# Performance work log

Measured on AMD Instinct MI355X. Metric: run time of the kernel, lower is better.

The kernel has to match this reference:

```python
import jax, jax.numpy as jnp
import numpy as np

N_NODES = 50000
N_EDGES = 800000
D_IN = 128
D_OUT = 128


def setup_inputs() -> dict:
    key = jax.random.key(0)
    k1, k2, k3, k4, k5 = jax.random.split(key, 5)
    x = jax.random.normal(k1, (N_NODES, D_IN), dtype=jnp.float32)
    w = jax.random.normal(k2, (D_IN, D_OUT), dtype=jnp.float32) * (1.0 / np.sqrt(D_IN))
    adj_rows = jnp.sort(jax.random.randint(k3, (N_EDGES,), 0, N_NODES, dtype=jnp.int32))
    adj_cols = jax.random.randint(k4, (N_EDGES,), 0, N_NODES, dtype=jnp.int32)
    adj_vals = jax.random.uniform(k5, (N_EDGES,), dtype=jnp.float32)
    return {"x": x, "w": w, "adj_rows": adj_rows, "adj_cols": adj_cols, "adj_vals": adj_vals}


def reference(x, w, adj_rows, adj_cols, adj_vals):
    # dense feature transform: [N, D_in] @ [D_in, D_out] -> [N, D_out]
    h = jnp.matmul(x, w)
    # sparse adjacency propagation (SpMM in COO form):
    # out[r] = sum over edges (r, c, v) of v * h[c]
    msg = adj_vals[:, None] * h[adj_cols]          # [E, D_out] gather
    out = jax.ops.segment_sum(msg, adj_rows, num_segments=x.shape[0])
    # activation (relu), fused into output pass
    return jax.nn.relu(out)
```

## Files before the change

### kernel.cpp

```cpp
#include <hip/hip_runtime.h>
#include <hip/hip_bf16.h>

#define D 128
#define GEMM_ROWS 32

typedef __bf16 bf16x8 __attribute__((ext_vector_type(8)));
typedef float  f32x4  __attribute__((ext_vector_type(4)));
typedef unsigned int u32x4 __attribute__((ext_vector_type(4)));

__global__ void transpose_w(const float* __restrict__ w, unsigned short* __restrict__ wT) {
    int idx = blockIdx.x * 256 + threadIdx.x;
    float v = w[idx];
    int k = idx >> 7, c = idx & 127;
    wT[c * D + k] = __builtin_bit_cast(unsigned short, (__bf16)v);
}

__global__ void build_row_ptr(const int* __restrict__ rows, int* __restrict__ row_ptr,
                              int n_edges, int n_nodes) {
    int e = blockIdx.x * 256 + threadIdx.x;
    if (e >= n_edges) return;
    int r    = rows[e];
    int prev = (e == 0) ? -1 : rows[e - 1];
    for (int rr = prev + 1; rr <= r; ++rr) row_ptr[rr] = e;
    if (e == n_edges - 1)
        for (int rr = r + 1; rr <= n_nodes; ++rr) row_ptr[rr] = n_edges;
}

__device__ inline bf16x8 load_a_frag(const float* __restrict__ x, int r, int koff, int n) {
    float4 v0 = make_float4(0.f, 0.f, 0.f, 0.f), v1 = v0;
    if (r < n) {
        const float4* p = (const float4*)(x + (size_t)r * D + koff);
        v0 = p[0]; v1 = p[1];
    }
    bf16x8 a;
    a[0] = (__bf16)v0.x; a[1] = (__bf16)v0.y; a[2] = (__bf16)v0.z; a[3] = (__bf16)v0.w;
    a[4] = (__bf16)v1.x; a[5] = (__bf16)v1.y; a[6] = (__bf16)v1.z; a[7] = (__bf16)v1.w;
    return a;
}

__global__ __launch_bounds__(256) void gemm_mfma2(const float* __restrict__ x,
                                                  const unsigned short* __restrict__ wT,
                                                  unsigned short* __restrict__ h, int n) {
    const int wave = threadIdx.x >> 6;
    const int lane = threadIdx.x & 63;
    const int m16  = lane & 15;
    const int q    = lane >> 4;

    const int row0 = blockIdx.x * 64;
    const int col0 = wave * 32;

    const u32x4* wTv = (const u32x4*)wT;
    bf16x8 bfr[2][4];
#pragma unroll
    for (int t = 0; t < 2; ++t)
#pragma unroll
        for (int s = 0; s < 4; ++s) {
            int ncol = col0 + 16 * t + m16;
            int koff = 32 * s + q * 8;
            bfr[t][s] = __builtin_bit_cast(bf16x8, wTv[(ncol * D + koff) >> 3]);
        }

    f32x4 acc[4][2];
#pragma unroll
    for (int sl = 0; sl < 4; ++sl)
#pragma unroll
        for (int t = 0; t < 2; ++t) acc[sl][t] = (f32x4)0.f;

#pragma unroll
    for (int sl = 0; sl < 4; ++sl) {
#pragma unroll
        for (int s = 0; s < 4; ++s) {
            bf16x8 a = load_a_frag(x, row0 + sl * 16 + m16, 32 * s + q * 8, n);
            acc[sl][0] = __builtin_amdgcn_mfma_f32_16x16x32_bf16(a, bfr[0][s], acc[sl][0], 0, 0, 0);
            acc[sl][1] = __builtin_amdgcn_mfma_f32_16x16x32_bf16(a, bfr[1][s], acc[sl][1], 0, 0, 0);
        }
    }

#pragma unroll
    for (int sl = 0; sl < 4; ++sl)
#pragma unroll
        for (int t = 0; t < 2; ++t) {
            int col = col0 + 16 * t + m16;
#pragma unroll
            for (int i = 0; i < 4; ++i) {
                int row = row0 + sl * 16 + q * 4 + i;
                if (row < n)
                    h[(size_t)row * D + col] =
                        __builtin_bit_cast(unsigned short, (__bf16)acc[sl][t][i]);
            }
        }
}

__global__ __launch_bounds__(256) void spmm_bf16(const unsigned short* __restrict__ h,
                                                 const int* __restrict__ row_ptr,
                                                 const int* __restrict__ cols,
                                                 const float* __restrict__ vals,
                                                 float* __restrict__ out, int n) {
    const int wave = threadIdx.x >> 6;
    const int lane = threadIdx.x & 63;
    const int r = blockIdx.x * 4 + wave;
    if (r >= n) return;

    const int start = row_ptr[r];
    const int end   = row_ptr[r + 1];
    const int chain = lane >> 4;
    const int l4    = lane & 15;

    const u32x4* h4 = (const u32x4*)h;
    float acc[8];
#pragma unroll
    for (int j = 0; j < 8; ++j) acc[j] = 0.f;

    int e = start + chain;
    int c = 0; float v = 0.f;
    if (e < end) { c = cols[e]; v = vals[e]; }
    while (e < end) {
        int en = e + 4; int cn = 0; float vn = 0.f;
        if (en < end) { cn = cols[en]; vn = vals[en]; }
        u32x4 hv = h4[(size_t)c * (D / 8) + l4];
#pragma unroll
        for (int j = 0; j < 4; ++j) {
            unsigned int u = hv[j];
            float lo = __builtin_bit_cast(float, u << 16);
            float hi = __builtin_bit_cast(float, u & 0xFFFF0000u);
            acc[2 * j]     = fmaf(v, lo, acc[2 * j]);
            acc[2 * j + 1] = fmaf(v, hi, acc[2 * j + 1]);
        }
        c = cn; v = vn; e = en;
    }

#pragma unroll
    for (int j = 0; j < 8; ++j) {
        acc[j] += __shfl_xor(acc[j], 16);
        acc[j] += __shfl_xor(acc[j], 32);
    }

    if (chain == 0) {
        float4 o0, o1;
        o0.x = fmaxf(acc[0], 0.f); o0.y = fmaxf(acc[1], 0.f);
        o0.z = fmaxf(acc[2], 0.f); o0.w = fmaxf(acc[3], 0.f);
        o1.x = fmaxf(acc[4], 0.f); o1.y = fmaxf(acc[5], 0.f);
        o1.z = fmaxf(acc[6], 0.f); o1.w = fmaxf(acc[7], 0.f);
        float4* op = (float4*)(out + (size_t)r * D + l4 * 8);
        op[0] = o0; op[1] = o1;
    }
}

__global__ __launch_bounds__(256) void gemm128(const float* __restrict__ x,
                                               const float* __restrict__ w,
                                               float* __restrict__ h, int n) {
    __shared__ float4 ws4[D * D / 4];
    __shared__ float  xs[GEMM_ROWS][D];
    const int tid  = threadIdx.x;
    const int row0 = blockIdx.x * GEMM_ROWS;
    const float4* w4 = (const float4*)w;
    for (int i = tid; i < D * D / 4; i += 256) ws4[i] = w4[i];
    float4* xs4 = (float4*)&xs[0][0];
    const float4* x4 = (const float4*)x;
    for (int i = tid; i < GEMM_ROWS * D / 4; i += 256) {
        int row = row0 + (i >> 5);
        float4 v = make_float4(0.f, 0.f, 0.f, 0.f);
        if (row < n) v = x4[(size_t)row0 * (D / 4) + i];
        xs4[i] = v;
    }
    __syncthreads();
    const int tx = tid & 31, ty = tid >> 5;
    float4 acc[4];
#pragma unroll
    for (int i = 0; i < 4; ++i) acc[i] = make_float4(0.f, 0.f, 0.f, 0.f);
#pragma unroll 8
    for (int k = 0; k < D; ++k) {
        float4 wv = ws4[k * (D / 4) + tx];
#pragma unroll
        for (int i = 0; i < 4; ++i) {
            float xv = xs[ty * 4 + i][k];
            acc[i].x = fmaf(xv, wv.x, acc[i].x);
            acc[i].y = fmaf(xv, wv.y, acc[i].y);
            acc[i].z = fmaf(xv, wv.z, acc[i].z);
            acc[i].w = fmaf(xv, wv.w, acc[i].w);
        }
    }
#pragma unroll
    for (int i = 0; i < 4; ++i) {
        int row = row0 + ty * 4 + i;
        if (row < n) ((float4*)(h + (size_t)row * D))[tx] = acc[i];
    }
}

__global__ __launch_bounds__(128) void spmm_row(const float* __restrict__ h,
                                                const int* __restrict__ rows,
                                                const int* __restrict__ cols,
                                                const float* __restrict__ vals,
                                                float* __restrict__ out, int n_edges) {
    const int r = blockIdx.x, d = threadIdx.x;
    int lo = 0, hi = n_edges;
    while (lo < hi) { int m = (lo + hi) >> 1; if (rows[m] < r) lo = m + 1; else hi = m; }
    const int start = lo;
    hi = n_edges;
    while (lo < hi) { int m = (lo + hi) >> 1; if (rows[m] <= r) lo = m + 1; else hi = m; }
    const int end = lo;
    float acc = 0.f;
    for (int e = start; e < end; ++e)
        acc = fmaf(vals[e], h[(size_t)cols[e] * D + d], acc);
    out[(size_t)r * D + d] = fmaxf(acc, 0.f);
}

__global__ __launch_bounds__(128) void fused_fallback(
        const float* __restrict__ x, const float* __restrict__ w,
        const int* __restrict__ rows, const int* __restrict__ cols,
        const float* __restrict__ vals, float* __restrict__ out, int n_edges) {
    const int r = blockIdx.x, d = threadIdx.x;
    int lo = 0, hi = n_edges;
    while (lo < hi) { int m = (lo + hi) >> 1; if (rows[m] < r) lo = m + 1; else hi = m; }
    const int start = lo;
    hi = n_edges;
    while (lo < hi) { int m = (lo + hi) >> 1; if (rows[m] <= r) lo = m + 1; else hi = m; }
    const int end = lo;
    float acc = 0.f;
    for (int e = start; e < end; ++e) {
        int c = cols[e]; float v = vals[e];
        float hcd = 0.f;
        for (int k = 0; k < D; ++k)
            hcd = fmaf(x[(size_t)c * D + k], w[(size_t)k * D + d], hcd);
        acc = fmaf(v, hcd, acc);
    }
    out[(size_t)r * D + d] = fmaxf(acc, 0.f);
}

extern "C" void kernel_launch(void* const* d_in, const int* in_sizes, int n_in,
                              void* d_out, int out_size, void* d_ws, size_t ws_size,
                              hipStream_t stream) {
    const float* x    = (const float*)d_in[0];
    const float* w    = (const float*)d_in[1];
    const int*   rows = (const int*)d_in[2];
    const int*   cols = (const int*)d_in[3];
    const float* vals = (const float*)d_in[4];
    float* out = (float*)d_out;

    const int n_nodes = in_sizes[0] / D;
    const int n_edges = in_sizes[2];

    const size_t hb_bytes = (size_t)n_nodes * D * sizeof(unsigned short);
    const size_t wT_off   = (hb_bytes + 15) & ~(size_t)15;
    const size_t rp_off   = wT_off + (size_t)D * D * sizeof(unsigned short);
    const size_t need     = rp_off + (size_t)(n_nodes + 1) * sizeof(int);
    const size_t hf_bytes = (size_t)n_nodes * D * sizeof(float);

    if (ws_size >= need) {
        unsigned short* h  = (unsigned short*)d_ws;
        unsigned short* wT = (unsigned short*)((char*)d_ws + wT_off);
        int*            rp = (int*)((char*)d_ws + rp_off);

        transpose_w<<<(D * D) / 256, 256, 0, stream>>>(w, wT);
        build_row_ptr<<<(n_edges + 255) / 256, 256, 0, stream>>>(rows, rp, n_edges, n_nodes);
        gemm_mfma2<<<(n_nodes + 63) / 64, 256, 0, stream>>>(x, wT, h, n_nodes);
        spmm_bf16<<<(n_nodes + 3) / 4, 256, 0, stream>>>(h, rp, cols, vals, out, n_nodes);
    } else if (ws_size >= hf_bytes) {
        float* h = (float*)d_ws;
        gemm128<<<(n_nodes + GEMM_ROWS - 1) / GEMM_ROWS, 256, 0, stream>>>(x, w, h, n_nodes);
        spmm_row<<<n_nodes, 128, 0, stream>>>(h, rows, cols, vals, out, n_edges);
    } else {
        fused_fallback<<<n_nodes, 128, 0, stream>>>(x, w, rows, cols, vals, out, n_edges);
    }
}
```

Before: 138.3 us.

## Merge preprocessing kernels and pre-convert x to padded bf16 for GEMM

Merges the weight transpose and row-pointer build into one launch, which also converts x to a padded bf16 copy. The GEMM then reads bf16 A fragments directly and drops its row bounds checks. The aim is to cut launch count and halve the GEMM's A-operand reads. In exchange it adds a full extra pass that reads x in fp32 and writes it back as bf16, and it needs more workspace.

```diff
diff --git a/kernel.cpp b/kernel.cpp
--- a/kernel.cpp
+++ b/kernel.cpp
@@ -8,39 +8,55 @@
 typedef float  f32x4  __attribute__((ext_vector_type(4)));
 typedef unsigned int u32x4 __attribute__((ext_vector_type(4)));
 
-__global__ void transpose_w(const float* __restrict__ w, unsigned short* __restrict__ wT) {
-    int idx = blockIdx.x * 256 + threadIdx.x;
-    float v = w[idx];
-    int k = idx >> 7, c = idx & 127;
-    wT[c * D + k] = __builtin_bit_cast(unsigned short, (__bf16)v);
-}
-
-__global__ void build_row_ptr(const int* __restrict__ rows, int* __restrict__ row_ptr,
-                              int n_edges, int n_nodes) {
-    int e = blockIdx.x * 256 + threadIdx.x;
-    if (e >= n_edges) return;
-    int r    = rows[e];
-    int prev = (e == 0) ? -1 : rows[e - 1];
-    for (int rr = prev + 1; rr <= r; ++rr) row_ptr[rr] = e;
-    if (e == n_edges - 1)
-        for (int rr = r + 1; rr <= n_nodes; ++rr) row_ptr[rr] = n_edges;
-}
-
-__device__ inline bf16x8 load_a_frag(const float* __restrict__ x, int r, int koff, int n) {
-    float4 v0 = make_float4(0.f, 0.f, 0.f, 0.f), v1 = v0;
-    if (r < n) {
-        const float4* p = (const float4*)(x + (size_t)r * D + koff);
-        v0 = p[0]; v1 = p[1];
-    }
-    bf16x8 a;
-    a[0] = (__bf16)v0.x; a[1] = (__bf16)v0.y; a[2] = (__bf16)v0.z; a[3] = (__bf16)v0.w;
-    a[4] = (__bf16)v1.x; a[5] = (__bf16)v1.y; a[6] = (__bf16)v1.z; a[7] = (__bf16)v1.w;
-    return a;
-}
-
-__global__ __launch_bounds__(256) void gemm_mfma2(const float* __restrict__ x,
-                                                  const unsigned short* __restrict__ wT,
-                                                  unsigned short* __restrict__ h, int n) {
+__device__ inline unsigned int pk_bf16(float lo, float hi) {
+    unsigned short a = __builtin_bit_cast(unsigned short, (__bf16)lo);
+    unsigned short b = __builtin_bit_cast(unsigned short, (__bf16)hi);
+    return ((unsigned int)b << 16) | (unsigned int)a;
+}
+
+__global__ __launch_bounds__(256) void preprocess(
+        const float* __restrict__ x, const float* __restrict__ w,
+        const int* __restrict__ rows,
+        unsigned short* __restrict__ xb, unsigned short* __restrict__ wT,
+        int* __restrict__ rp,
+        int n_nodes, int n_pad, int n_edges, int xb_blocks, int w_blocks) {
+    const int b = blockIdx.x;
+    if (b < xb_blocks) {
+        int t = b * 256 + threadIdx.x;
+        int row = t >> 4, chunk = t & 15;
+        if (row >= n_pad) return;
+        u32x4 o = (u32x4)0u;
+        if (row < n_nodes) {
+            const float4* p = (const float4*)(x + (size_t)row * D + chunk * 8);
+            float4 v0 = p[0], v1 = p[1];
+            o[0] = pk_bf16(v0.x, v0.y); o[1] = pk_bf16(v0.z, v0.w);
+            o[2] = pk_bf16(v1.x, v1.y); o[3] = pk_bf16(v1.z, v1.w);
+        }
+        ((u32x4*)xb)[t] = o;
+    } else if (b < xb_blocks + w_blocks) {
+        int t = (b - xb_blocks) * 256 + threadIdx.x;
+#pragma unroll
+        for (int j = 0; j < 8; ++j) {
+            int idx = t * 8 + j;
+            float v = w[idx];
+            int k = idx >> 7, c = idx & 127;
+            wT[c * D + k] = __builtin_bit_cast(unsigned short, (__bf16)v);
+        }
+    } else {
+        int e = (b - xb_blocks - w_blocks) * 256 + threadIdx.x;
+        if (e >= n_edges) return;
+        int r    = rows[e];
+        int prev = (e == 0) ? -1 : rows[e - 1];
+        for (int rr = prev + 1; rr <= r; ++rr) rp[rr] = e;
+        if (e == n_edges - 1)
+            for (int rr = r + 1; rr <= n_nodes; ++rr) rp[rr] = n_edges;
+    }
+}
+
+__global__ __launch_bounds__(256) void gemm_v3(const unsigned short* __restrict__ xb,
+                                               const unsigned short* __restrict__ wT,
+                                               unsigned short* __restrict__ h,
+                                               int n_pad) {
     const int wave = threadIdx.x >> 6;
     const int lane = threadIdx.x & 63;
     const int m16  = lane & 15;
@@ -49,7 +65,9 @@
     const int row0 = blockIdx.x * 64;
     const int col0 = wave * 32;
 
+    const u32x4* xbv = (const u32x4*)xb;
     const u32x4* wTv = (const u32x4*)wT;
+
     bf16x8 bfr[2][4];
 #pragma unroll
     for (int t = 0; t < 2; ++t)
@@ -68,9 +86,10 @@
 
 #pragma unroll
     for (int sl = 0; sl < 4; ++sl) {
+        const size_t rbase = (size_t)(row0 + sl * 16 + m16) * D;
 #pragma unroll
         for (int s = 0; s < 4; ++s) {
-            bf16x8 a = load_a_frag(x, row0 + sl * 16 + m16, 32 * s + q * 8, n);
+            bf16x8 a = __builtin_bit_cast(bf16x8, xbv[(rbase + 32 * s + q * 8) >> 3]);
             acc[sl][0] = __builtin_amdgcn_mfma_f32_16x16x32_bf16(a, bfr[0][s], acc[sl][0], 0, 0, 0);
             acc[sl][1] = __builtin_amdgcn_mfma_f32_16x16x32_bf16(a, bfr[1][s], acc[sl][1], 0, 0, 0);
         }
@@ -84,9 +103,8 @@
 #pragma unroll
             for (int i = 0; i < 4; ++i) {
                 int row = row0 + sl * 16 + q * 4 + i;
-                if (row < n)
-                    h[(size_t)row * D + col] =
-                        __builtin_bit_cast(unsigned short, (__bf16)acc[sl][t][i]);
+                h[(size_t)row * D + col] =
+                    __builtin_bit_cast(unsigned short, (__bf16)acc[sl][t][i]);
             }
         }
 }
@@ -239,26 +257,33 @@
 
     const int n_nodes = in_sizes[0] / D;
     const int n_edges = in_sizes[2];
-
-    const size_t hb_bytes = (size_t)n_nodes * D * sizeof(unsigned short);
-    const size_t wT_off   = (hb_bytes + 15) & ~(size_t)15;
+    const int n_pad   = (n_nodes + 63) & ~63;
+
+    const size_t xb_bytes = (size_t)n_pad * D * sizeof(unsigned short);
+    const size_t h_off    = xb_bytes;
+    const size_t wT_off   = h_off + xb_bytes;
     const size_t rp_off   = wT_off + (size_t)D * D * sizeof(unsigned short);
     const size_t need     = rp_off + (size_t)(n_nodes + 1) * sizeof(int);
     const size_t hf_bytes = (size_t)n_nodes * D * sizeof(float);
 
     if (ws_size >= need) {
-        unsigned short* h  = (unsigned short*)d_ws;
+        unsigned short* xb = (unsigned short*)d_ws;
+        unsigned short* h  = (unsigned short*)((char*)d_ws + h_off);
         unsigned short* wT = (unsigned short*)((char*)d_ws + wT_off);
         int*            rp = (int*)((char*)d_ws + rp_off);
 
-        transpose_w<<<(D * D) / 256, 256, 0, stream>>>(w, wT);
-        build_row_ptr<<<(n_edges + 255) / 256, 256, 0, stream>>>(rows, rp, n_edges, n_nodes);
-        gemm_mfma2<<<(n_nodes + 63) / 64, 256, 0, stream>>>(x, wT, h, n_nodes);
+        const int xb_blocks = (n_pad * (D / 8)) / 256;
+        const int w_blocks  = (D * D) / (256 * 8);
+        const int rp_blocks = (n_edges + 255) / 256;
+        preprocess<<<xb_blocks + w_blocks + rp_blocks, 256, 0, stream>>>(
+            x, w, rows, xb, wT, rp, n_nodes, n_pad, n_edges, xb_blocks, w_blocks);
+
+        gemm_v3<<<n_pad / 64, 256, 0, stream>>>(xb, wT, h, n_pad);
         spmm_bf16<<<(n_nodes + 3) / 4, 256, 0, stream>>>(h, rp, cols, vals, out, n_nodes);
     } else if (ws_size >= hf_bytes) {
-        float* h = (float*)d_ws;
-        gemm128<<<(n_nodes + GEMM_ROWS - 1) / GEMM_ROWS, 256, 0, stream>>>(x, w, h, n_nodes);
-        spmm_row<<<n_nodes, 128, 0, stream>>>(h, rows, cols, vals, out, n_edges);
+        float* hf = (float*)d_ws;
+        gemm128<<<(n_nodes + GEMM_ROWS - 1) / GEMM_ROWS, 256, 0, stream>>>(x, w, hf, n_nodes);
+        spmm_row<<<n_nodes, 128, 0, stream>>>(hf, rows, cols, vals, out, n_edges);
     } else {
         fused_fallback<<<n_nodes, 128, 0, stream>>>(x, w, rows, cols, vals, out, n_edges);
     }
```

New measurement: 133.8 us. 1.03x faster.

## Fuse weight transpose, row-pointer build and GEMM into one launch

Applied to the files above, without the earlier changes.

Merges the transpose_w, build_row_ptr and gemm_mfma2 kernels into a single launch. The first blocks do the MFMA GEMM and the trailing blocks build the CSR row pointers. Each GEMM block now reads W directly as strided fp32 and converts it to bf16 itself, instead of reading a pre-transposed bf16 copy. The row-slice loop is no longer unrolled, so each slice is stored right after it is computed, and h is padded to a multiple of 64 rows so the store bounds checks can go. This removes two kernel launches and their serialization, but every block now does uncoalesced strided W loads, which may cost more.

```diff
diff --git a/kernel.cpp b/kernel.cpp
--- a/kernel.cpp
+++ b/kernel.cpp
@@ -8,87 +8,81 @@
 typedef float  f32x4  __attribute__((ext_vector_type(4)));
 typedef unsigned int u32x4 __attribute__((ext_vector_type(4)));
 
-__global__ void transpose_w(const float* __restrict__ w, unsigned short* __restrict__ wT) {
-    int idx = blockIdx.x * 256 + threadIdx.x;
-    float v = w[idx];
-    int k = idx >> 7, c = idx & 127;
-    wT[c * D + k] = __builtin_bit_cast(unsigned short, (__bf16)v);
-}
-
-__global__ void build_row_ptr(const int* __restrict__ rows, int* __restrict__ row_ptr,
-                              int n_edges, int n_nodes) {
-    int e = blockIdx.x * 256 + threadIdx.x;
-    if (e >= n_edges) return;
-    int r    = rows[e];
-    int prev = (e == 0) ? -1 : rows[e - 1];
-    for (int rr = prev + 1; rr <= r; ++rr) row_ptr[rr] = e;
-    if (e == n_edges - 1)
-        for (int rr = r + 1; rr <= n_nodes; ++rr) row_ptr[rr] = n_edges;
-}
-
-__device__ inline bf16x8 load_a_frag(const float* __restrict__ x, int r, int koff, int n) {
-    float4 v0 = make_float4(0.f, 0.f, 0.f, 0.f), v1 = v0;
-    if (r < n) {
-        const float4* p = (const float4*)(x + (size_t)r * D + koff);
-        v0 = p[0]; v1 = p[1];
-    }
+__device__ inline bf16x8 cvt_a8(const float* __restrict__ p) {
+    float4 v0 = ((const float4*)p)[0], v1 = ((const float4*)p)[1];
     bf16x8 a;
     a[0] = (__bf16)v0.x; a[1] = (__bf16)v0.y; a[2] = (__bf16)v0.z; a[3] = (__bf16)v0.w;
     a[4] = (__bf16)v1.x; a[5] = (__bf16)v1.y; a[6] = (__bf16)v1.z; a[7] = (__bf16)v1.w;
     return a;
 }
 
-__global__ __launch_bounds__(256) void gemm_mfma2(const float* __restrict__ x,
-                                                  const unsigned short* __restrict__ wT,
-                                                  unsigned short* __restrict__ h, int n) {
+__global__ __launch_bounds__(256) void fused_gemm_rp(
+        const float* __restrict__ x, const float* __restrict__ w,
+        const int* __restrict__ rows,
+        unsigned short* __restrict__ h, int* __restrict__ rp,
+        int n_nodes, int n_edges, int gemm_blocks) {
+    const int b = blockIdx.x;
+
+    if (b >= gemm_blocks) {
+        int e = (b - gemm_blocks) * 256 + threadIdx.x;
+        if (e >= n_edges) return;
+        int r    = rows[e];
+        int prev = (e == 0) ? -1 : rows[e - 1];
+        for (int rr = prev + 1; rr <= r; ++rr) rp[rr] = e;
+        if (e == n_edges - 1)
+            for (int rr = r + 1; rr <= n_nodes; ++rr) rp[rr] = n_edges;
+        return;
+    }
+
     const int wave = threadIdx.x >> 6;
     const int lane = threadIdx.x & 63;
     const int m16  = lane & 15;
     const int q    = lane >> 4;
 
-    const int row0 = blockIdx.x * 64;
+    const int row0 = b * 64;
     const int col0 = wave * 32;
 
-    const u32x4* wTv = (const u32x4*)wT;
     bf16x8 bfr[2][4];
 #pragma unroll
     for (int t = 0; t < 2; ++t)
 #pragma unroll
         for (int s = 0; s < 4; ++s) {
-            int ncol = col0 + 16 * t + m16;
-            int koff = 32 * s + q * 8;
-            bfr[t][s] = __builtin_bit_cast(bf16x8, wTv[(ncol * D + koff) >> 3]);
-        }
-
-    f32x4 acc[4][2];
-#pragma unroll
-    for (int sl = 0; sl < 4; ++sl)
-#pragma unroll
-        for (int t = 0; t < 2; ++t) acc[sl][t] = (f32x4)0.f;
-
-#pragma unroll
+            const float* wp = w + (size_t)(32 * s + q * 8) * D + col0 + 16 * t + m16;
+#pragma unroll
+            for (int j = 0; j < 8; ++j)
+                bfr[t][s][j] = (__bf16)wp[(size_t)j * D];
+        }
+
+#pragma unroll 1
     for (int sl = 0; sl < 4; ++sl) {
+        const int r = row0 + sl * 16 + m16;
+        const float* xp = x + (size_t)r * D + q * 8;
+
+        bf16x8 a[4];
+        if (r < n_nodes) {
+#pragma unroll
+            for (int s = 0; s < 4; ++s) a[s] = cvt_a8(xp + 32 * s);
+        } else {
+#pragma unroll
+            for (int s = 0; s < 4; ++s)
+#pragma unroll
+                for (int j = 0; j < 8; ++j) a[s][j] = (__bf16)0.f;
+        }
+
+        f32x4 acc0 = (f32x4)0.f, acc1 = (f32x4)0.f;
 #pragma unroll
         for (int s = 0; s < 4; ++s) {
-            bf16x8 a = load_a_frag(x, row0 + sl * 16 + m16, 32 * s + q * 8, n);
-            acc[sl][0] = __builtin_amdgcn_mfma_f32_16x16x32_bf16(a, bfr[0][s], acc[sl][0], 0, 0, 0);
-            acc[sl][1] = __builtin_amdgcn_mfma_f32_16x16x32_bf16(a, bfr[1][s], acc[sl][1], 0, 0, 0);
-        }
-    }
-
-#pragma unroll
-    for (int sl = 0; sl < 4; ++sl)
-#pragma unroll
-        for (int t = 0; t < 2; ++t) {
-            int col = col0 + 16 * t + m16;
-#pragma unroll
-            for (int i = 0; i < 4; ++i) {
-                int row = row0 + sl * 16 + q * 4 + i;
-                if (row < n)
-                    h[(size_t)row * D + col] =
-                        __builtin_bit_cast(unsigned short, (__bf16)acc[sl][t][i]);
-            }
-        }
+            acc0 = __builtin_amdgcn_mfma_f32_16x16x32_bf16(a[s], bfr[0][s], acc0, 0, 0, 0);
+            acc1 = __builtin_amdgcn_mfma_f32_16x16x32_bf16(a[s], bfr[1][s], acc1, 0, 0, 0);
+        }
+
+#pragma unroll
+        for (int i = 0; i < 4; ++i) {
+            int row = row0 + sl * 16 + q * 4 + i;
+            h[(size_t)row * D + col0 + m16]      = __builtin_bit_cast(unsigned short, (__bf16)acc0[i]);
+            h[(size_t)row * D + col0 + 16 + m16] = __builtin_bit_cast(unsigned short, (__bf16)acc1[i]);
+        }
+    }
 }
 
 __global__ __launch_bounds__(256) void spmm_bf16(const unsigned short* __restrict__ h,
@@ -239,26 +233,26 @@
 
     const int n_nodes = in_sizes[0] / D;
     const int n_edges = in_sizes[2];
-
-    const size_t hb_bytes = (size_t)n_nodes * D * sizeof(unsigned short);
-    const size_t wT_off   = (hb_bytes + 15) & ~(size_t)15;
-    const size_t rp_off   = wT_off + (size_t)D * D * sizeof(unsigned short);
+    const int n_pad   = (n_nodes + 63) & ~63;
+
+    const size_t h_bytes  = (size_t)n_pad * D * sizeof(unsigned short);
+    const size_t rp_off   = h_bytes;
     const size_t need     = rp_off + (size_t)(n_nodes + 1) * sizeof(int);
     const size_t hf_bytes = (size_t)n_nodes * D * sizeof(float);
 
     if (ws_size >= need) {
         unsigned short* h  = (unsigned short*)d_ws;
-        unsigned short* wT = (unsigned short*)((char*)d_ws + wT_off);
         int*            rp = (int*)((char*)d_ws + rp_off);
 
-        transpose_w<<<(D * D) / 256, 256, 0, stream>>>(w, wT);
-        build_row_ptr<<<(n_edges + 255) / 256, 256, 0, stream>>>(rows, rp, n_edges, n_nodes);
-        gemm_mfma2<<<(n_nodes + 63) / 64, 256, 0, stream>>>(x, wT, h, n_nodes);
+        const int gemm_blocks = n_pad / 64;
+        const int rp_blocks   = (n_edges + 255) / 256;
+        fused_gemm_rp<<<gemm_blocks + rp_blocks, 256, 0, stream>>>(
+            x, w, rows, h, rp, n_nodes, n_edges, gemm_blocks);
         spmm_bf16<<<(n_nodes + 3) / 4, 256, 0, stream>>>(h, rp, cols, vals, out, n_nodes);
     } else if (ws_size >= hf_bytes) {
-        float* h = (float*)d_ws;
-        gemm128<<<(n_nodes + GEMM_ROWS - 1) / GEMM_ROWS, 256, 0, stream>>>(x, w, h, n_nodes);
-        spmm_row<<<n_nodes, 128, 0, stream>>>(h, rows, cols, vals, out, n_edges);
+        float* hf = (float*)d_ws;
+        gemm128<<<(n_nodes + GEMM_ROWS - 1) / GEMM_ROWS, 256, 0, stream>>>(x, w, hf, n_nodes);
+        spmm_row<<<n_nodes, 128, 0, stream>>>(hf, rows, cols, vals, out, n_edges);
     } else {
         fused_fallback<<<n_nodes, 128, 0, stream>>>(x, w, rows, cols, vals, out, n_edges);
     }
```

Result: faster. 131.4 us (-5.0%).
